# Kernel tuning notes

Measured on AMD Instinct MI355X. Metric: run time of the kernel, lower is better.

Reference implementation:

```python
import jax, jax.numpy as jnp
import numpy as np

B, S, E = 4, 2048, 1024
H, HD, R = 16, 64, 32  # heads, head_dim, rank


def setup_inputs() -> dict:
    key = jax.random.key(0)
    ks = jax.random.split(key, 9)
    sc = 0.02
    return {
        "hidden_states": jax.random.normal(ks[0], (B, S, E), jnp.float32),
        "q_weight": jax.random.normal(ks[1], (E, E), jnp.float32) * sc,
        "q_bias": jax.random.normal(ks[2], (E,), jnp.float32) * sc,
        "k_weight": jax.random.normal(ks[3], (E, E), jnp.float32) * sc,
        "k_bias": jax.random.normal(ks[4], (E,), jnp.float32) * sc,
        "low_rank_value_weight": jax.random.normal(ks[5], (E, H * R), jnp.float32) * sc,
        "low_rank_value_bias": jax.random.normal(ks[6], (H * R,), jnp.float32) * sc,
        "low_rank_output_weight": jax.random.normal(ks[7], (H * R, E), jnp.float32) * sc,
        "output_bias": jax.random.normal(ks[8], (E,), jnp.float32) * sc,
    }


def reference(hidden_states, q_weight, q_bias, k_weight, k_bias,
              low_rank_value_weight, low_rank_value_bias,
              low_rank_output_weight, output_bias):
    b, s, _ = hidden_states.shape
    q = hidden_states @ q_weight + q_bias                       # [B,S,E]
    k = hidden_states @ k_weight + k_bias                       # [B,S,E]
    v = hidden_states @ low_rank_value_weight + low_rank_value_bias  # [B,S,H*R]
    q = q.reshape(b, s, H, HD).transpose(0, 2, 1, 3)            # [B,H,S,HD]
    k = k.reshape(b, s, H, HD).transpose(0, 2, 1, 3)
    v = v.reshape(b, s, H, R).transpose(0, 2, 1, 3)             # [B,H,S,R]
    scores = jnp.einsum('bhqd,bhkd->bhqk', q, k) / jnp.sqrt(jnp.float32(HD))
    causal = jnp.tril(jnp.ones((s, s), dtype=bool))
    scores = jnp.where(causal, scores, jnp.finfo(scores.dtype).min)
    probs = jax.nn.softmax(scores, axis=-1)                     # [B,H,S,S]
    attn = jnp.einsum('bhqk,bhkr->bhqr', probs, v)              # [B,H,S,R]
    attn = attn.transpose(0, 2, 1, 3).reshape(b, s, H * R)      # [B,S,H*R]
    out = attn @ low_rank_output_weight + output_bias           # [B,S,E]
    return out
```

## Files before the change

kernel.cpp:

```cpp
#include <hip/hip_runtime.h>

typedef _Float16 f16;
typedef __attribute__((ext_vector_type(4))) float f4;
typedef __attribute__((ext_vector_type(4))) _Float16 h4;
typedef __attribute__((ext_vector_type(8))) _Float16 h8;
typedef __attribute__((ext_vector_type(4))) float f32x4;
typedef __attribute__((ext_vector_type(4))) unsigned int u4;

extern "C" __device__ __attribute__((const)) float __ocml_native_exp2_f32(float);
#define EXP2F __ocml_native_exp2_f32
#define L2E 1.4426950408889634f

#define SWZ(row, colByte) \
  (((row) << 7) + ((colByte) ^ (((((row) ^ ((row) >> 3))) & 7) << 4)))

#define GL16(gp, lp)                                                  \
  __builtin_amdgcn_global_load_lds(                                   \
      (const __attribute__((address_space(1))) unsigned int*)(gp),    \
      (__attribute__((address_space(3))) unsigned int*)(lp), 16, 0, 0)

__global__ __launch_bounds__(256) void prep(
    const float* __restrict__ hs, f16* __restrict__ hsf,
    const float* __restrict__ qw, const float* __restrict__ kw,
    const float* __restrict__ vw, const float* __restrict__ ow,
    f16* __restrict__ wqkv, f16* __restrict__ owt) {
  const int t = threadIdx.x;
  if (blockIdx.x < 2048) {
    const int n4 = 8192 * 1024 / 4;
    for (int i = blockIdx.x * 256 + t; i < n4; i += 2048 * 256) {
      const f4 v = ((const f4*)hs)[i];
      h4 h;
      h.x = (f16)v.x; h.y = (f16)v.y; h.z = (f16)v.z; h.w = (f16)v.w;
      ((h4*)hsf)[i] = h;
    }
    return;
  }
  __shared__ float tile[32][33];
  int bid = blockIdx.x - 2048;
  const float* in;
  f16* out;
  int R, C, bx, by;
  if (bid < 1024) {
    in = qw; out = wqkv; R = 1024; C = 1024; bx = bid & 31; by = bid >> 5;
  } else if (bid < 2048) {
    bid -= 1024;
    in = kw; out = wqkv + (size_t)1024 * 1024; R = 1024; C = 1024;
    bx = bid & 31; by = bid >> 5;
  } else if (bid < 2560) {
    bid -= 2048;
    in = vw; out = wqkv + (size_t)2048 * 1024; R = 1024; C = 512;
    bx = bid & 15; by = bid >> 4;
  } else {
    bid -= 2560;
    in = ow; out = owt; R = 512; C = 1024; bx = bid & 31; by = bid >> 5;
  }
  const int tx = t & 31, ty = t >> 5;
  const int bc = bx * 32, br = by * 32;
#pragma unroll
  for (int i = 0; i < 4; ++i)
    tile[ty + i * 8][tx] = in[(size_t)(br + ty + i * 8) * C + bc + tx];
  __syncthreads();
#pragma unroll
  for (int i = 0; i < 4; ++i)
    out[(size_t)(bc + ty + i * 8) * R + br + tx] = (f16)tile[tx][ty + i * 8];
}

__global__ __launch_bounds__(256) void hgemm_qkv(
    const f16* __restrict__ A, const f16* __restrict__ Bt,
    const float* __restrict__ qb, const float* __restrict__ kb,
    const float* __restrict__ vb,
    f16* __restrict__ qf, f16* __restrict__ kf, f16* __restrict__ vf) {
  __shared__ f16 As[2 * 128 * 32];
  __shared__ f16 Bs[2 * 128 * 32];
  const int K = 1024;
  const int id = blockIdx.x;
  const int xcd = id & 7, loc = id >> 3;
  const int grp = loc >> 5, inn = loc & 31;
  const int bnT = grp * 4 + (inn >> 3);
  const int bm = (xcd * 8 + (inn & 7)) * 128;
  const int bn = bnT * 128;
  const int t = threadIdx.x;
  const int lane = t & 63, wave = t >> 6;
  const int wr = wave >> 1, wc = wave & 1;
  const int lrow = lane & 15, lk = lane >> 4;
  const int srow = lane >> 2;
  const int sblk = (lane & 3) ^ ((srow ^ (srow >> 2)) & 3);

  f32x4 acc[4][4];
#pragma unroll
  for (int i = 0; i < 4; ++i)
#pragma unroll
    for (int j = 0; j < 4; ++j) acc[i][j] = (f32x4)0.f;

  auto stage = [&](int buf, int ktile) {
#pragma unroll
    for (int i = 0; i < 2; ++i) {
      const int rr = (wave * 2 + i) * 16 + srow;
      GL16(A + (size_t)(bm + rr) * K + ktile * 32 + sblk * 8,
           (char*)As + buf * 8192 + (wave * 2 + i) * 1024);
      GL16(Bt + (size_t)(bn + rr) * K + ktile * 32 + sblk * 8,
           (char*)Bs + buf * 8192 + (wave * 2 + i) * 1024);
    }
  };

  stage(0, 0);
  for (int kt = 0; kt < 32; ++kt) {
    const int cur = kt & 1;
    stage(cur ^ 1, (kt + 1) & 31);
    asm volatile("s_waitcnt vmcnt(4)" ::: "memory");
    __builtin_amdgcn_s_barrier();
    __builtin_amdgcn_sched_barrier(0);
    h8 af[4], bf[4];
#pragma unroll
    for (int f = 0; f < 4; ++f) {
      const int ra = wr * 64 + f * 16 + lrow;
      af[f] = *(const h8*)((char*)As + cur * 8192 + ra * 64 +
                           ((lk ^ ((ra ^ (ra >> 2)) & 3)) << 4));
      const int rb = wc * 64 + f * 16 + lrow;
      bf[f] = *(const h8*)((char*)Bs + cur * 8192 + rb * 64 +
                           ((lk ^ ((rb ^ (rb >> 2)) & 3)) << 4));
    }
#pragma unroll
    for (int i2 = 0; i2 < 4; ++i2)
#pragma unroll
      for (int j = 0; j < 4; ++j)
        acc[i2][j] = __builtin_amdgcn_mfma_f32_16x16x32_f16(af[i2], bf[j], acc[i2][j], 0, 0, 0);
    asm volatile("s_waitcnt lgkmcnt(0)" ::: "memory");
    __builtin_amdgcn_sched_barrier(0);
    __builtin_amdgcn_s_barrier();
  }

  const float* bias;
  int nbase;
  if (bnT < 8) { bias = qb; nbase = 0; }
  else if (bnT < 16) { bias = kb; nbase = 1024; }
  else { bias = vb; nbase = 2048; }

#pragma unroll
  for (int fi = 0; fi < 4; ++fi) {
#pragma unroll
    for (int j = 0; j < 4; ++j) {
      const int grow = bm + wr * 64 + fi * 16 + lk * 4 + j;
      const int bb = grow >> 11, ss = grow & 2047;
#pragma unroll
      for (int fj = 0; fj < 4; ++fj) {
        const int gcol = bn + wc * 64 + fj * 16 + lrow;
        const int nl = gcol - nbase;
        const float g = acc[fi][fj][j] + bias[nl];
        if (bnT < 8) {
          qf[((size_t)(bb * 16 + (nl >> 6)) * 2048 + ss) * 64 + (nl & 63)] = (f16)g;
        } else if (bnT < 16) {
          kf[((size_t)(bb * 16 + (nl >> 6)) * 2048 + ss) * 64 + (nl & 63)] = (f16)g;
        } else {
          vf[((size_t)(bb * 16 + (nl >> 5)) * 2048 + ss) * 32 + (nl & 31)] = (f16)g;
        }
      }
    }
  }
}

__global__ __launch_bounds__(256) void transpose_v(
    const f16* __restrict__ vf, f16* __restrict__ vfT) {
  __shared__ f16 tl[32][36];
  const int bh = blockIdx.x >> 6;
  const int st = (blockIdx.x & 63) * 32;
  const int t = threadIdx.x;
  const int row = t >> 3, cq = t & 7;
  {
    const h4 v = *(const h4*)(vf + ((size_t)bh * 2048 + st + row) * 32 + cq * 4);
    *(h4*)&tl[row][cq * 4] = v;
  }
  __syncthreads();
  {
    h4 v;
#pragma unroll
    for (int e = 0; e < 4; ++e) v[e] = tl[cq * 4 + e][row];
    *(h4*)(vfT + ((size_t)bh * 32 + row) * 2048 + st + cq * 4) = v;
  }
}

__global__ __launch_bounds__(256) void hgemm_out(
    const f16* __restrict__ A, const f16* __restrict__ Bt,
    const float* __restrict__ bias, float* __restrict__ outp,
    const int N, const int K) {
  __shared__ f16 As[128 * 40];
  __shared__ f16 Bs[128 * 40];
  const int id = blockIdx.x;
  const int swz = (id & 7) * 64 + (id >> 3);
  const int bn = (swz & 7) * 128;
  const int bm = (swz >> 3) * 128;
  const int t = threadIdx.x;
  const int lane = t & 63, wave = t >> 6;
  const int wr = wave >> 1, wc = wave & 1;
  const int lrow = lane & 15, lk = lane >> 4;

  f32x4 acc[4][4];
#pragma unroll
  for (int i = 0; i < 4; ++i)
#pragma unroll
    for (int j = 0; j < 4; ++j) acc[i][j] = (f32x4)0.f;

  for (int kt = 0; kt < K; kt += 32) {
#pragma unroll
    for (int i = 0; i < 2; ++i) {
      const int ch = t + i * 256;
      const int row = ch >> 2, part = ch & 3;
      *(u4*)&As[row * 40 + part * 8] =
          *(const u4*)(A + (size_t)(bm + row) * K + kt + part * 8);
      *(u4*)&Bs[row * 40 + part * 8] =
          *(const u4*)(Bt + (size_t)(bn + row) * K + kt + part * 8);
    }
    __syncthreads();
    h8 af[4], bf[4];
#pragma unroll
    for (int f = 0; f < 4; ++f) {
      af[f] = *(const h8*)&As[(wr * 64 + f * 16 + lrow) * 40 + lk * 8];
      bf[f] = *(const h8*)&Bs[(wc * 64 + f * 16 + lrow) * 40 + lk * 8];
    }
#pragma unroll
    for (int i = 0; i < 4; ++i)
#pragma unroll
      for (int j = 0; j < 4; ++j)
        acc[i][j] = __builtin_amdgcn_mfma_f32_16x16x32_f16(af[i], bf[j], acc[i][j], 0, 0, 0);
    __syncthreads();
  }

#pragma unroll
  for (int fi = 0; fi < 4; ++fi) {
#pragma unroll
    for (int j = 0; j < 4; ++j) {
      const int grow = bm + wr * 64 + fi * 16 + lk * 4 + j;
#pragma unroll
      for (int fj = 0; fj < 4; ++fj) {
        const int gcol = bn + wc * 64 + fj * 16 + lrow;
        outp[(size_t)grow * N + gcol] = acc[fi][fj][j] + bias[gcol];
      }
    }
  }
}

__global__ __launch_bounds__(256) void attn_mfma(
    const f16* __restrict__ qf, const f16* __restrict__ kf,
    const f16* __restrict__ vfT, f16* __restrict__ attf) {
  __shared__ f16 Ks[64 * 64];
  __shared__ f16 VsT[32 * 64];
  __shared__ f16 Ps[4 * 32 * 64];
  const int id = blockIdx.x;
  const int bh = id & 63;
  const int qblk = 15 - (id >> 6);
  const int qbase = qblk * 128;
  const int t = threadIdx.x;
  const int lane = t & 63, w = t >> 6;
  const int l15 = lane & 15, g = lane >> 4;
  const size_t kvbase = (size_t)bh * 2048;
  char* Pw = (char*)&Ps[w * 32 * 64];

  h8 ones;
#pragma unroll
  for (int e = 0; e < 8; ++e) ones[e] = (f16)1.0f;

  h8 qreg[2][2];
#pragma unroll
  for (int fj = 0; fj < 2; ++fj) {
    const int q = qbase + fj * 64 + w * 16 + l15;
#pragma unroll
    for (int ks = 0; ks < 2; ++ks) {
      h8 raw = *(const h8*)(qf + (kvbase + q) * 64 + ks * 32 + g * 8);
#pragma unroll
      for (int e = 0; e < 8; ++e) raw[e] = raw[e] * (f16)0.125f;
      qreg[fj][ks] = raw;
    }
  }

  f32x4 accO[2][2];
  f32x4 accL[2];
#pragma unroll
  for (int i = 0; i < 2; ++i) {
    accL[i] = (f32x4)0.f;
#pragma unroll
    for (int j = 0; j < 2; ++j) accO[i][j] = (f32x4)0.f;
  }
  float m2[2] = {-1.0e30f, -1.0e30f};

  const int ntiles = qblk * 2 + 2;
  for (int kt = 0; kt < ntiles; ++kt) {
    const int kbase = kt * 64;
    __syncthreads();
#pragma unroll
    for (int i = 0; i < 2; ++i) {
      const int idx = t + i * 256;
      const int row = idx >> 3, ch = idx & 7;
      *(u4*)((char*)Ks + SWZ(row, ch * 16)) =
          *(const u4*)(kf + (kvbase + kbase + row) * 64 + ch * 8);
    }
    {
      const int row = t >> 3, ch = t & 7;
      *(u4*)((char*)VsT + SWZ(row, ch * 16)) =
          *(const u4*)(vfT + ((size_t)bh * 32 + row) * 2048 + kbase + ch * 8);
    }
    __syncthreads();

    f32x4 accS[4][2];
#pragma unroll
    for (int i = 0; i < 4; ++i)
#pragma unroll
      for (int j = 0; j < 2; ++j) accS[i][j] = (f32x4)0.f;
#pragma unroll
    for (int ks = 0; ks < 2; ++ks) {
#pragma unroll
      for (int fim = 0; fim < 4; ++fim) {
        const h8 af = *(const h8*)((char*)Ks + SWZ(fim * 16 + l15, ks * 64 + g * 16));
#pragma unroll
        for (int fj = 0; fj < 2; ++fj)
          accS[fim][fj] = __builtin_amdgcn_mfma_f32_16x16x32_f16(af, qreg[fj][ks], accS[fim][fj], 0, 0, 0);
      }
    }

#pragma unroll
    for (int fj = 0; fj < 2; ++fj) {
      const int qg = qbase + fj * 64 + w * 16 + l15;
      const bool need_mask = (kbase + 63 > qbase + fj * 64 + w * 16);
      float sc[4][4];
#pragma unroll
      for (int fim = 0; fim < 4; ++fim)
#pragma unroll
        for (int j = 0; j < 4; ++j) {
          float v = accS[fim][fj][j];
          if (need_mask) {
            const int key = kbase + fim * 16 + g * 4 + j;
            v = (key <= qg) ? v : -1.0e30f;
          }
          sc[fim][j] = v;
        }
      const float a0 = fmaxf(fmaxf(sc[0][0], sc[0][1]), sc[0][2]);
      const float a1 = fmaxf(fmaxf(sc[0][3], sc[1][0]), sc[1][1]);
      const float a2 = fmaxf(fmaxf(sc[1][2], sc[1][3]), sc[2][0]);
      const float a3 = fmaxf(fmaxf(sc[2][1], sc[2][2]), sc[2][3]);
      const float a4 = fmaxf(fmaxf(sc[3][0], sc[3][1]), sc[3][2]);
      float mc = fmaxf(fmaxf(fmaxf(a0, a1), a2),
                       fmaxf(fmaxf(a3, a4), sc[3][3]));
      mc = fmaxf(mc, __shfl_xor(mc, 16));
      mc = fmaxf(mc, __shfl_xor(mc, 32));
      if (!__all(mc <= m2[fj] + 1.5f)) {
        const float mnew = fmaxf(m2[fj], mc);
        const float corr = __expf(m2[fj] - mnew);
        m2[fj] = mnew;
#pragma unroll
        for (int j = 0; j < 4; ++j) {
          const float c = __shfl(corr, g * 4 + j);
          accO[fj][0][j] *= c;
          accO[fj][1][j] *= c;
          accL[fj][j] *= c;
        }
      }
      const float nml = -m2[fj] * L2E;
#pragma unroll
      for (int fim = 0; fim < 4; ++fim) {
        h4 hp;
#pragma unroll
        for (int j = 0; j < 4; ++j)
          hp[j] = (f16)EXP2F(fmaf(sc[fim][j], L2E, nml));
        *(h4*)(Pw + SWZ(fj * 16 + l15, fim * 32 + g * 8)) = hp;
      }
    }

#pragma unroll
    for (int ks = 0; ks < 2; ++ks) {
      const h8 pa0 = *(const h8*)(Pw + SWZ(l15, ks * 64 + g * 16));
      const h8 pa1 = *(const h8*)(Pw + SWZ(16 + l15, ks * 64 + g * 16));
#pragma unroll
      for (int fr = 0; fr < 2; ++fr) {
        const h8 vb = *(const h8*)((char*)VsT + SWZ(fr * 16 + l15, ks * 64 + g * 16));
        accO[0][fr] = __builtin_amdgcn_mfma_f32_16x16x32_f16(pa0, vb, accO[0][fr], 0, 0, 0);
        accO[1][fr] = __builtin_amdgcn_mfma_f32_16x16x32_f16(pa1, vb, accO[1][fr], 0, 0, 0);
      }
      accL[0] = __builtin_amdgcn_mfma_f32_16x16x32_f16(pa0, ones, accL[0], 0, 0, 0);
      accL[1] = __builtin_amdgcn_mfma_f32_16x16x32_f16(pa1, ones, accL[1], 0, 0, 0);
    }
  }

  const int b = bh >> 4, h = bh & 15;
#pragma unroll
  for (int fo = 0; fo < 2; ++fo) {
#pragma unroll
    for (int j = 0; j < 4; ++j) {
      const float iv = 1.f / accL[fo][j];
      const int q = qbase + fo * 64 + w * 16 + g * 4 + j;
#pragma unroll
      for (int fr = 0; fr < 2; ++fr) {
        const int r = fr * 16 + l15;
        attf[((size_t)b * 2048 + q) * 512 + h * 32 + r] = (f16)(accO[fo][fr][j] * iv);
      }
    }
  }
}

extern "C" void kernel_launch(void* const* d_in, const int* in_sizes, int n_in,
                              void* d_out, int out_size, void* d_ws, size_t ws_size,
                              hipStream_t stream) {
  const float* hs = (const float*)d_in[0];
  const float* qw = (const float*)d_in[1];
  const float* qb = (const float*)d_in[2];
  const float* kw = (const float*)d_in[3];
  const float* kb = (const float*)d_in[4];
  const float* vw = (const float*)d_in[5];
  const float* vb = (const float*)d_in[6];
  const float* ow = (const float*)d_in[7];
  const float* ob = (const float*)d_in[8];
  float* out = (float*)d_out;
  char* ws = (char*)d_ws;

  f16* qf = (f16*)(ws);
  f16* kf = (f16*)(ws + ((size_t)16 << 20));
  f16* vf = (f16*)(ws + ((size_t)32 << 20));
  f16* vfT = (f16*)(ws + ((size_t)72 << 20));
  f16* attf = (f16*)(ws + ((size_t)40 << 20));
  f16* wqkv = (f16*)(ws + ((size_t)48 << 20));
  f16* owt = (f16*)(ws + ((size_t)53 << 20));
  f16* hsf = (f16*)(ws + ((size_t)56 << 20));

  prep<<<dim3(5120), 256, 0, stream>>>(hs, hsf, qw, kw, vw, ow, wqkv, owt);
  hgemm_qkv<<<dim3(1280), 256, 0, stream>>>(hsf, wqkv, qb, kb, vb, qf, kf, vf);
  transpose_v<<<dim3(4096), 256, 0, stream>>>(vf, vfT);
  attn_mfma<<<dim3(1024), 256, 0, stream>>>(qf, kf, vfT, attf);
  hgemm_out<<<dim3(512), 256, 0, stream>>>(attf, owt, ob, out, 1024, 512);
}
```

Baseline: 162.8 us.

## Pair causal q-blocks per workgroup and double-buffer K/V tiles via registers

The attention kernel now launches half as many workgroups. Each one processes two query blocks (qblk = 15-p and p), so every workgroup does the same amount of causal work. K/V tiles are double-buffered in LDS: the next tile is prefetched into registers while the current one is computed, then stored into the alternate buffer, leaving one barrier per tile instead of two. This costs more LDS and registers, and the smaller grid gives fewer workgroups to spread across the CUs.

```diff
diff --git a/kernel.cpp b/kernel.cpp
--- a/kernel.cpp
+++ b/kernel.cpp
@@ -242,156 +242,179 @@
 __global__ __launch_bounds__(256) void attn_mfma(
     const f16* __restrict__ qf, const f16* __restrict__ kf,
     const f16* __restrict__ vfT, f16* __restrict__ attf) {
-  __shared__ f16 Ks[64 * 64];
-  __shared__ f16 VsT[32 * 64];
+  __shared__ f16 Ks[2][64 * 64];
+  __shared__ f16 VsT[2][32 * 64];
   __shared__ f16 Ps[4 * 32 * 64];
   const int id = blockIdx.x;
   const int bh = id & 63;
-  const int qblk = 15 - (id >> 6);
-  const int qbase = qblk * 128;
+  const int p = id >> 6;
   const int t = threadIdx.x;
   const int lane = t & 63, w = t >> 6;
   const int l15 = lane & 15, g = lane >> 4;
   const size_t kvbase = (size_t)bh * 2048;
   char* Pw = (char*)&Ps[w * 32 * 64];
+  const int srow = t >> 3, sch = t & 7;
+  const int b = bh >> 4, h = bh & 15;
 
   h8 ones;
 #pragma unroll
   for (int e = 0; e < 8; ++e) ones[e] = (f16)1.0f;
 
-  h8 qreg[2][2];
-#pragma unroll
-  for (int fj = 0; fj < 2; ++fj) {
-    const int q = qbase + fj * 64 + w * 16 + l15;
-#pragma unroll
-    for (int ks = 0; ks < 2; ++ks) {
-      h8 raw = *(const h8*)(qf + (kvbase + q) * 64 + ks * 32 + g * 8);
-#pragma unroll
-      for (int e = 0; e < 8; ++e) raw[e] = raw[e] * (f16)0.125f;
-      qreg[fj][ks] = raw;
-    }
-  }
-
-  f32x4 accO[2][2];
-  f32x4 accL[2];
-#pragma unroll
-  for (int i = 0; i < 2; ++i) {
-    accL[i] = (f32x4)0.f;
-#pragma unroll
-    for (int j = 0; j < 2; ++j) accO[i][j] = (f32x4)0.f;
-  }
-  float m2[2] = {-1.0e30f, -1.0e30f};
-
-  const int ntiles = qblk * 2 + 2;
-  for (int kt = 0; kt < ntiles; ++kt) {
-    const int kbase = kt * 64;
+#pragma unroll
+  for (int run = 0; run < 2; ++run) {
+    const int qblk = run ? p : 15 - p;
+    const int qbase = qblk * 128;
+
+    h8 qreg[2][2];
+#pragma unroll
+    for (int fj = 0; fj < 2; ++fj) {
+      const int q = qbase + fj * 64 + w * 16 + l15;
+#pragma unroll
+      for (int ks = 0; ks < 2; ++ks) {
+        h8 raw = *(const h8*)(qf + (kvbase + q) * 64 + ks * 32 + g * 8);
+#pragma unroll
+        for (int e = 0; e < 8; ++e) raw[e] = raw[e] * (f16)0.125f;
+        qreg[fj][ks] = raw;
+      }
+    }
+
+    f32x4 accO[2][2];
+    f32x4 accL[2];
+#pragma unroll
+    for (int i = 0; i < 2; ++i) {
+      accL[i] = (f32x4)0.f;
+#pragma unroll
+      for (int j = 0; j < 2; ++j) accO[i][j] = (f32x4)0.f;
+    }
+    float m2[2] = {-1.0e30f, -1.0e30f};
+
+    const int ntiles = qblk * 2 + 2;
+
+    {
+      const u4 k0 = *(const u4*)(kf + (kvbase + srow) * 64 + sch * 8);
+      const u4 k1 = *(const u4*)(kf + (kvbase + 32 + srow) * 64 + sch * 8);
+      const u4 v0 = *(const u4*)(vfT + ((size_t)bh * 32 + srow) * 2048 + sch * 8);
+      *(u4*)((char*)&Ks[0][0] + SWZ(srow, sch * 16)) = k0;
+      *(u4*)((char*)&Ks[0][0] + SWZ(srow + 32, sch * 16)) = k1;
+      *(u4*)((char*)&VsT[0][0] + SWZ(srow, sch * 16)) = v0;
+    }
     __syncthreads();
-#pragma unroll
-    for (int i = 0; i < 2; ++i) {
-      const int idx = t + i * 256;
-      const int row = idx >> 3, ch = idx & 7;
-      *(u4*)((char*)Ks + SWZ(row, ch * 16)) =
-          *(const u4*)(kf + (kvbase + kbase + row) * 64 + ch * 8);
-    }
-    {
-      const int row = t >> 3, ch = t & 7;
-      *(u4*)((char*)VsT + SWZ(row, ch * 16)) =
-          *(const u4*)(vfT + ((size_t)bh * 32 + row) * 2048 + kbase + ch * 8);
+
+    u4 kr0, kr1, vr0;
+    for (int kt = 0; kt < ntiles; ++kt) {
+      const int cur = kt & 1;
+      const int kbase = kt * 64;
+      const bool more = (kt + 1 < ntiles);
+      if (more) {
+        const int kb2 = kbase + 64;
+        kr0 = *(const u4*)(kf + (kvbase + kb2 + srow) * 64 + sch * 8);
+        kr1 = *(const u4*)(kf + (kvbase + kb2 + 32 + srow) * 64 + sch * 8);
+        vr0 = *(const u4*)(vfT + ((size_t)bh * 32 + srow) * 2048 + kb2 + sch * 8);
+      }
+
+      f32x4 accS[4][2];
+#pragma unroll
+      for (int i = 0; i < 4; ++i)
+#pragma unroll
+        for (int j = 0; j < 2; ++j) accS[i][j] = (f32x4)0.f;
+#pragma unroll
+      for (int ks = 0; ks < 2; ++ks) {
+#pragma unroll
+        for (int fim = 0; fim < 4; ++fim) {
+          const h8 af = *(const h8*)((char*)&Ks[cur][0] +
+                                     SWZ(fim * 16 + l15, ks * 64 + g * 16));
+#pragma unroll
+          for (int fj = 0; fj < 2; ++fj)
+            accS[fim][fj] = __builtin_amdgcn_mfma_f32_16x16x32_f16(
+                af, qreg[fj][ks], accS[fim][fj], 0, 0, 0);
+        }
+      }
+
+#pragma unroll
+      for (int fj = 0; fj < 2; ++fj) {
+        const int qg = qbase + fj * 64 + w * 16 + l15;
+        const bool need_mask = (kbase + 63 > qbase + fj * 64 + w * 16);
+        float sc[4][4];
+#pragma unroll
+        for (int fim = 0; fim < 4; ++fim)
+#pragma unroll
+          for (int j = 0; j < 4; ++j) {
+            float v = accS[fim][fj][j];
+            if (need_mask) {
+              const int key = kbase + fim * 16 + g * 4 + j;
+              v = (key <= qg) ? v : -1.0e30f;
+            }
+            sc[fim][j] = v;
+          }
+        const float a0 = fmaxf(fmaxf(sc[0][0], sc[0][1]), sc[0][2]);
+        const float a1 = fmaxf(fmaxf(sc[0][3], sc[1][0]), sc[1][1]);
+        const float a2 = fmaxf(fmaxf(sc[1][2], sc[1][3]), sc[2][0]);
+        const float a3 = fmaxf(fmaxf(sc[2][1], sc[2][2]), sc[2][3]);
+        const float a4 = fmaxf(fmaxf(sc[3][0], sc[3][1]), sc[3][2]);
+        float mc = fmaxf(fmaxf(fmaxf(a0, a1), a2),
+                         fmaxf(fmaxf(a3, a4), sc[3][3]));
+        mc = fmaxf(mc, __shfl_xor(mc, 16));
+        mc = fmaxf(mc, __shfl_xor(mc, 32));
+        if (!__all(mc <= m2[fj] + 1.5f)) {
+          const float mnew = fmaxf(m2[fj], mc);
+          const float corr = __expf(m2[fj] - mnew);
+          m2[fj] = mnew;
+#pragma unroll
+          for (int j = 0; j < 4; ++j) {
+            const float c = __shfl(corr, g * 4 + j);
+            accO[fj][0][j] *= c;
+            accO[fj][1][j] *= c;
+            accL[fj][j] *= c;
+          }
+        }
+        const float nml = -m2[fj] * L2E;
+#pragma unroll
+        for (int fim = 0; fim < 4; ++fim) {
+          h4 hp;
+#pragma unroll
+          for (int j = 0; j < 4; ++j)
+            hp[j] = (f16)EXP2F(fmaf(sc[fim][j], L2E, nml));
+          *(h4*)(Pw + SWZ(fj * 16 + l15, fim * 32 + g * 8)) = hp;
+        }
+      }
+
+#pragma unroll
+      for (int ks = 0; ks < 2; ++ks) {
+        const h8 pa0 = *(const h8*)(Pw + SWZ(l15, ks * 64 + g * 16));
+        const h8 pa1 = *(const h8*)(Pw + SWZ(16 + l15, ks * 64 + g * 16));
+#pragma unroll
+        for (int fr = 0; fr < 2; ++fr) {
+          const h8 vb = *(const h8*)((char*)&VsT[cur][0] +
+                                     SWZ(fr * 16 + l15, ks * 64 + g * 16));
+          accO[0][fr] = __builtin_amdgcn_mfma_f32_16x16x32_f16(pa0, vb, accO[0][fr], 0, 0, 0);
+          accO[1][fr] = __builtin_amdgcn_mfma_f32_16x16x32_f16(pa1, vb, accO[1][fr], 0, 0, 0);
+        }
+        accL[0] = __builtin_amdgcn_mfma_f32_16x16x32_f16(pa0, ones, accL[0], 0, 0, 0);
+        accL[1] = __builtin_amdgcn_mfma_f32_16x16x32_f16(pa1, ones, accL[1], 0, 0, 0);
+      }
+
+      if (more) {
+        *(u4*)((char*)&Ks[cur ^ 1][0] + SWZ(srow, sch * 16)) = kr0;
+        *(u4*)((char*)&Ks[cur ^ 1][0] + SWZ(srow + 32, sch * 16)) = kr1;
+        *(u4*)((char*)&VsT[cur ^ 1][0] + SWZ(srow, sch * 16)) = vr0;
+      }
+      __syncthreads();
+    }
+
+#pragma unroll
+    for (int fo = 0; fo < 2; ++fo) {
+#pragma unroll
+      for (int j = 0; j < 4; ++j) {
+        const float iv = 1.f / accL[fo][j];
+        const int q = qbase + fo * 64 + w * 16 + g * 4 + j;
+#pragma unroll
+        for (int fr = 0; fr < 2; ++fr) {
+          const int r = fr * 16 + l15;
+          attf[((size_t)b * 2048 + q) * 512 + h * 32 + r] = (f16)(accO[fo][fr][j] * iv);
+        }
+      }
     }
     __syncthreads();
-
-    f32x4 accS[4][2];
-#pragma unroll
-    for (int i = 0; i < 4; ++i)
-#pragma unroll
-      for (int j = 0; j < 2; ++j) accS[i][j] = (f32x4)0.f;
-#pragma unroll
-    for (int ks = 0; ks < 2; ++ks) {
-#pragma unroll
-      for (int fim = 0; fim < 4; ++fim) {
-        const h8 af = *(const h8*)((char*)Ks + SWZ(fim * 16 + l15, ks * 64 + g * 16));
-#pragma unroll
-        for (int fj = 0; fj < 2; ++fj)
-          accS[fim][fj] = __builtin_amdgcn_mfma_f32_16x16x32_f16(af, qreg[fj][ks], accS[fim][fj], 0, 0, 0);
-      }
-    }
-
-#pragma unroll
-    for (int fj = 0; fj < 2; ++fj) {
-      const int qg = qbase + fj * 64 + w * 16 + l15;
-      const bool need_mask = (kbase + 63 > qbase + fj * 64 + w * 16);
-      float sc[4][4];
-#pragma unroll
-      for (int fim = 0; fim < 4; ++fim)
-#pragma unroll
-        for (int j = 0; j < 4; ++j) {
-          float v = accS[fim][fj][j];
-          if (need_mask) {
-            const int key = kbase + fim * 16 + g * 4 + j;
-            v = (key <= qg) ? v : -1.0e30f;
-          }
-          sc[fim][j] = v;
-        }
-      const float a0 = fmaxf(fmaxf(sc[0][0], sc[0][1]), sc[0][2]);
-      const float a1 = fmaxf(fmaxf(sc[0][3], sc[1][0]), sc[1][1]);
-      const float a2 = fmaxf(fmaxf(sc[1][2], sc[1][3]), sc[2][0]);
-      const float a3 = fmaxf(fmaxf(sc[2][1], sc[2][2]), sc[2][3]);
-      const float a4 = fmaxf(fmaxf(sc[3][0], sc[3][1]), sc[3][2]);
-      float mc = fmaxf(fmaxf(fmaxf(a0, a1), a2),
-                       fmaxf(fmaxf(a3, a4), sc[3][3]));
-      mc = fmaxf(mc, __shfl_xor(mc, 16));
-      mc = fmaxf(mc, __shfl_xor(mc, 32));
-      if (!__all(mc <= m2[fj] + 1.5f)) {
-        const float mnew = fmaxf(m2[fj], mc);
-        const float corr = __expf(m2[fj] - mnew);
-        m2[fj] = mnew;
-#pragma unroll
-        for (int j = 0; j < 4; ++j) {
-          const float c = __shfl(corr, g * 4 + j);
-          accO[fj][0][j] *= c;
-          accO[fj][1][j] *= c;
-          accL[fj][j] *= c;
-        }
-      }
-      const float nml = -m2[fj] * L2E;
-#pragma unroll
-      for (int fim = 0; fim < 4; ++fim) {
-        h4 hp;
-#pragma unroll
-        for (int j = 0; j < 4; ++j)
-          hp[j] = (f16)EXP2F(fmaf(sc[fim][j], L2E, nml));
-        *(h4*)(Pw + SWZ(fj * 16 + l15, fim * 32 + g * 8)) = hp;
-      }
-    }
-
-#pragma unroll
-    for (int ks = 0; ks < 2; ++ks) {
-      const h8 pa0 = *(const h8*)(Pw + SWZ(l15, ks * 64 + g * 16));
-      const h8 pa1 = *(const h8*)(Pw + SWZ(16 + l15, ks * 64 + g * 16));
-#pragma unroll
-      for (int fr = 0; fr < 2; ++fr) {
-        const h8 vb = *(const h8*)((char*)VsT + SWZ(fr * 16 + l15, ks * 64 + g * 16));
-        accO[0][fr] = __builtin_amdgcn_mfma_f32_16x16x32_f16(pa0, vb, accO[0][fr], 0, 0, 0);
-        accO[1][fr] = __builtin_amdgcn_mfma_f32_16x16x32_f16(pa1, vb, accO[1][fr], 0, 0, 0);
-      }
-      accL[0] = __builtin_amdgcn_mfma_f32_16x16x32_f16(pa0, ones, accL[0], 0, 0, 0);
-      accL[1] = __builtin_amdgcn_mfma_f32_16x16x32_f16(pa1, ones, accL[1], 0, 0, 0);
-    }
-  }
-
-  const int b = bh >> 4, h = bh & 15;
-#pragma unroll
-  for (int fo = 0; fo < 2; ++fo) {
-#pragma unroll
-    for (int j = 0; j < 4; ++j) {
-      const float iv = 1.f / accL[fo][j];
-      const int q = qbase + fo * 64 + w * 16 + g * 4 + j;
-#pragma unroll
-      for (int fr = 0; fr < 2; ++fr) {
-        const int r = fr * 16 + l15;
-        attf[((size_t)b * 2048 + q) * 512 + h * 32 + r] = (f16)(accO[fo][fr][j] * iv);
-      }
-    }
   }
 }
 
@@ -422,6 +445,6 @@
   prep<<<dim3(5120), 256, 0, stream>>>(hs, hsf, qw, kw, vw, ow, wqkv, owt);
   hgemm_qkv<<<dim3(1280), 256, 0, stream>>>(hsf, wqkv, qb, kb, vb, qf, kf, vf);
   transpose_v<<<dim3(4096), 256, 0, stream>>>(vf, vfT);
-  attn_mfma<<<dim3(1024), 256, 0, stream>>>(qf, kf, vfT, attf);
+  attn_mfma<<<dim3(512), 256, 0, stream>>>(qf, kf, vfT, attf);
   hgemm_out<<<dim3(512), 256, 0, stream>>>(attf, owt, ob, out, 1024, 512);
 }
```

Measured after the change: 162.9 us. Within noise of the previous version (+0.1%).
